# Kernel tuning notes

Hardware: AMD Instinct MI355X
Metric: run time of the kernel (lower is better)

## Reference

```python
import jax, jax.numpy as jnp
import numpy as np

B, C, T, F = 4, 96, 320, 256
BN_EPS = 1e-5


def _cbp(x, W, b, gamma, beta, mean, var, a):
    """1x1 Conv2d + BatchNorm2d (inference stats) + PReLU (single param)."""
    y = jnp.einsum('oc,bctf->botf', W, x) + b[None, :, None, None]
    scale = gamma * jax.lax.rsqrt(var + BN_EPS)
    y = (y - mean[None, :, None, None]) * scale[None, :, None, None] + beta[None, :, None, None]
    return jnp.where(y >= 0, y, a * y)


def setup_inputs() -> dict:
    key = jax.random.key(0)
    ks = jax.random.split(key, 24)
    d = {"inp": jax.random.normal(ks[0], (B, C, T, F), dtype=jnp.float32)}

    def mk_params(i, cout):
        kk = jax.random.split(ks[i], 7)
        return dict(
            W=jax.random.normal(kk[0], (cout, C), dtype=jnp.float32) / np.sqrt(C),
            b=jnp.zeros((cout,), dtype=jnp.float32),
            gamma=jnp.ones((cout,), dtype=jnp.float32) + 0.1 * jax.random.normal(kk[1], (cout,), dtype=jnp.float32),
            beta=0.1 * jax.random.normal(kk[2], (cout,), dtype=jnp.float32),
            mean=0.1 * jax.random.normal(kk[3], (cout,), dtype=jnp.float32),
            var=jax.random.uniform(kk[4], (cout,), dtype=jnp.float32) + 0.5,
            a=jnp.float32(0.25),
        )

    for tag, i, cout in (("f", 1, 3 * C), ("t", 2, 2 * C), ("p", 3, C)):
        p = mk_params(i, cout)
        for k, v in p.items():
            d[k + "_" + tag] = v
    return d


def reference(inp,
              W_f, b_f, gamma_f, beta_f, mean_f, var_f, a_f,
              W_t, b_t, gamma_t, beta_t, mean_t, var_t, a_t,
              W_p, b_p, gamma_p, beta_p, mean_p, var_p, a_p):
    c = inp.shape[1]
    scale = 1.0 / jnp.sqrt(jnp.float32(c))

    # frequency-axis attention
    f_qkv = _cbp(inp, W_f, b_f, gamma_f, beta_f, mean_f, var_f, a_f)  # [B,3C,T,F]
    qf, kf, v = f_qkv[:, :c], f_qkv[:, c:2 * c], f_qkv[:, 2 * c:]
    f_score = jnp.einsum('bctf,bcty->btfy', qf, kf) * scale
    f_score = jax.nn.softmax(f_score, axis=-1)
    f_out = jnp.einsum('btfy,bcty->bctf', f_score, v)

    # time-axis attention (NOTE: original's masked_fill is non-inplace and
    # its result is discarded, so the causal mask has NO effect; replicated.)
    t_qk = _cbp(inp, W_t, b_t, gamma_t, beta_t, mean_t, var_t, a_t)  # [B,2C,T,F]
    qt, kt = t_qk[:, :c], t_qk[:, c:]
    t_score = jnp.einsum('bctf,bcyf->bfty', qt, kt) * scale
    t_score = jax.nn.softmax(t_score, axis=-1)
    t_out = jnp.einsum('bfty,bcyf->bctf', t_score, f_out)

    out = _cbp(t_out, W_p, b_p, gamma_p, beta_p, mean_p, var_p, a_p)
    return out + inp
```

## Files before the change

### kernel.cpp

```cpp
#include <hip/hip_runtime.h>
#include <math.h>

typedef float f4 __attribute__((ext_vector_type(4)));
typedef float f2 __attribute__((ext_vector_type(2)));
typedef float f32x4 __attribute__((ext_vector_type(4)));
typedef _Float16 h8 __attribute__((ext_vector_type(8)));

constexpr int B_ = 4, C_ = 96, T_ = 320, F_ = 256;
constexpr int TF_ = T_ * F_;
constexpr float EPS_ = 1e-5f;
constexpr size_t QH_ = (size_t)C_ * TF_;

constexpr int WPP = 92160, WTOT = 110592;

__global__ __launch_bounds__(256)
void prep_kernel(const float* __restrict__ Wf, const float* __restrict__ Wt,
                 const float* __restrict__ Wp,
                 const float* __restrict__ bf, const float* __restrict__ gf,
                 const float* __restrict__ bef, const float* __restrict__ mf,
                 const float* __restrict__ vf,
                 const float* __restrict__ bt, const float* __restrict__ gt,
                 const float* __restrict__ bet, const float* __restrict__ mt,
                 const float* __restrict__ vt,
                 const float* __restrict__ bp, const float* __restrict__ gp,
                 const float* __restrict__ bep, const float* __restrict__ mp,
                 const float* __restrict__ vp,
                 _Float16* __restrict__ wsp, float* __restrict__ scsh)
{
    const int gtid = blockIdx.x * 256 + threadIdx.x;
    const int gsz  = gridDim.x * 256;
    for (int i = gtid; i < 46080; i += gsz) {
        const int frid = i >> 9, le = i & 511;
        const int lane = le >> 3, j = le & 7;
        const int kk = frid % 3, m = (frid / 3) % 3,
                  wm = (frid / 9) & 1, cg = frid / 18;
        const int row = (wm * 3 + m) * 16 + (lane & 15);
        const int col = kk * 32 + (lane >> 4) * 8 + j;
        const float* src = (cg < 3) ? Wf + cg * 9216 : Wt + (cg - 3) * 9216;
        const float w = src[row * 96 + col];
        const _Float16 h = (_Float16)w;
        wsp[(frid * 2 + 0) * 512 + le] = h;
        wsp[(frid * 2 + 1) * 512 + le] = (_Float16)(w - (float)h);
    }
    for (int i = gtid; i < 9216; i += gsz) {
        const int frid = i >> 9, le = i & 511;
        const int lane = le >> 3, j = le & 7;
        const int kk = frid % 3, m = (frid / 3) % 3, wm = frid / 9;
        const int row = (wm * 3 + m) * 16 + (lane & 15);
        const int col = kk * 32 + (lane >> 4) * 8 + j;
        const float w = Wp[row * 96 + col];
        const _Float16 h = (_Float16)w;
        wsp[WPP + (frid * 2 + 0) * 512 + le] = h;
        wsp[WPP + (frid * 2 + 1) * 512 + le] = (_Float16)(w - (float)h);
    }
    if (gtid < 288) {
        const float sc = gf[gtid] * rsqrtf(vf[gtid] + EPS_);
        scsh[2 * gtid] = sc;
        scsh[2 * gtid + 1] = fmaf(bf[gtid] - mf[gtid], sc, bef[gtid]);
    } else if (gtid < 480) {
        const int i = gtid - 288;
        const float sc = gt[i] * rsqrtf(vt[i] + EPS_);
        scsh[576 + 2 * i] = sc;
        scsh[576 + 2 * i + 1] = fmaf(bt[i] - mt[i], sc, bet[i]);
    } else if (gtid < 576) {
        const int i = gtid - 480;
        const float sc = gp[i] * rsqrtf(vp[i] + EPS_);
        scsh[960 + 2 * i] = sc;
        scsh[960 + 2 * i + 1] = fmaf(bp[i] - mp[i], sc, bep[i]);
    }
}

__global__ __launch_bounds__(256, 3)
void conv_ft(const float* __restrict__ x, const _Float16* __restrict__ wsp,
             const float* __restrict__ scsh,
             const float* __restrict__ aPf, const float* __restrict__ aPt,
             _Float16* __restrict__ yf, _Float16* __restrict__ yt,
             int bsx, int bsyf, int bsyt)
{
    constexpr int LS = 200;
    extern __shared__ _Float16 ldsh[];
    _Float16* Xs0 = ldsh;
    _Float16* Xs1 = ldsh + 64 * LS;

    x  += (size_t)blockIdx.y * bsx;
    yf += (size_t)blockIdx.y * bsyf;
    yt += (size_t)blockIdx.y * bsyt;

    const int tid = threadIdx.x;
    const int p0A = blockIdx.x * 128;
    const int p0B = p0A + 64;

    {
        const float* xg = x + p0A;
        for (int e = tid; e < 64 * 12; e += 256) {
            const int p = e & 63, k0 = (e >> 6) * 8;
            const float* xp = xg + (size_t)k0 * TF_ + p;
            h8 hv, lv;
#pragma unroll
            for (int j = 0; j < 8; ++j) {
                const float xv = xp[(size_t)j * TF_];
                const _Float16 xh = (_Float16)xv;
                hv[j] = xh;
                lv[j] = (_Float16)(xv - (float)xh);
            }
            *(h8*)&Xs0[p * LS + k0]      = hv;
            *(h8*)&Xs0[p * LS + 96 + k0] = lv;
        }
    }

    const int lane = tid & 63, wid = tid >> 6;
    const int l16 = lane & 15, lg = lane >> 4;
    const int wm = wid >> 1, wn = wid & 1;
    const float af_ = aPf[0], at_ = aPt[0];
    __syncthreads();

    float xpre[3][8];
#pragma unroll
    for (int it = 0; it < 3; ++it) {
        const int e = tid + it * 256;
        const int p = e & 63, k0 = (e >> 6) * 8;
        const float* xp = x + p0B + (size_t)k0 * TF_ + p;
#pragma unroll
        for (int j = 0; j < 8; ++j) xpre[it][j] = xp[(size_t)j * TF_];
    }

    auto compute5 = [&](const _Float16* Xs, int p0) {
#pragma unroll 1
        for (int cg = 0; cg < 5; ++cg) {
            const float* ss; float a; _Float16* yo;
            if (cg < 3) {
                ss = scsh + cg * 192;        a = af_;
                yo = yf + (size_t)cg * QH_;
            } else {
                ss = scsh + 576 + (cg - 3) * 192;  a = at_;
                yo = yt + (size_t)(cg - 3) * QH_;
            }
            const _Float16* wbase = wsp + (size_t)(cg * 2 + wm) * 9 * 1024 + lane * 8;

            f32x4 acc[3][2];
#pragma unroll
            for (int m = 0; m < 3; ++m)
#pragma unroll
                for (int n = 0; n < 2; ++n) acc[m][n] = (f32x4){0.f, 0.f, 0.f, 0.f};

#pragma unroll
            for (int kk = 0; kk < 3; ++kk) {
                h8 bfh[2], bfl[2];
#pragma unroll
                for (int n = 0; n < 2; ++n) {
                    const int prow = (wn * 2 + n) * 16 + l16;
                    bfh[n] = *(const h8*)&Xs[prow * LS + kk * 32 + lg * 8];
                    bfl[n] = *(const h8*)&Xs[prow * LS + 96 + kk * 32 + lg * 8];
                }
#pragma unroll
                for (int m = 0; m < 3; ++m) {
                    const _Float16* wr = wbase + (size_t)(m * 3 + kk) * 1024;
                    const h8 wh = *(const h8*)&wr[0];
                    const h8 wl = *(const h8*)&wr[512];
#pragma unroll
                    for (int n = 0; n < 2; ++n) {
                        acc[m][n] = __builtin_amdgcn_mfma_f32_16x16x32_f16(wh, bfh[n], acc[m][n], 0, 0, 0);
                        acc[m][n] = __builtin_amdgcn_mfma_f32_16x16x32_f16(wl, bfh[n], acc[m][n], 0, 0, 0);
                        acc[m][n] = __builtin_amdgcn_mfma_f32_16x16x32_f16(wh, bfl[n], acc[m][n], 0, 0, 0);
                    }
                }
            }

#pragma unroll
            for (int m = 0; m < 3; ++m) {
#pragma unroll
                for (int r = 0; r < 4; ++r) {
                    const int col = (wm * 3 + m) * 16 + lg * 4 + r;
                    const f2 sp = *(const f2*)&ss[2 * col];
                    _Float16* yr = yo + (size_t)col * TF_ + p0 + wn * 32 + l16;
#pragma unroll
                    for (int n = 0; n < 2; ++n) {
                        const float v = fmaf(acc[m][n][r], sp[0], sp[1]);
                        yr[n * 16] = (_Float16)(v >= 0.f ? v : a * v);
                    }
                }
            }
        }
    };

    compute5(Xs0, p0A);

#pragma unroll
    for (int it = 0; it < 3; ++it) {
        const int e = tid + it * 256;
        const int p = e & 63, k0 = (e >> 6) * 8;
        h8 hv, lv;
#pragma unroll
        for (int j = 0; j < 8; ++j) {
            const _Float16 xh = (_Float16)xpre[it][j];
            hv[j] = xh;
            lv[j] = (_Float16)(xpre[it][j] - (float)xh);
        }
        *(h8*)&Xs1[p * LS + k0]      = hv;
        *(h8*)&Xs1[p * LS + 96 + k0] = lv;
    }
    __syncthreads();

    compute5(Xs1, p0B);
}

__device__ __forceinline__ void tr64_body(const _Float16* __restrict__ in,
                                          _Float16* __restrict__ out,
                                          int Mo, int No, int n0, int m0,
                                          _Float16* tile)
{
    const int t = threadIdx.x, ty = t >> 3, tx8 = t & 7;
#pragma unroll
    for (int r = 0; r < 2; ++r) {
        const int n = ty + r * 32;
        const h8 v = *(const h8*)&in[(size_t)(n0 + n) * Mo + m0 + tx8 * 8];
        const int c = tx8 ^ (n >> 3);
        *(h8*)&tile[n * 72 + c * 8] = v;
    }
    __syncthreads();
#pragma unroll
    for (int r = 0; r < 2; ++r) {
        const int mt = ty + r * 32;
        h8 v;
#pragma unroll
        for (int j = 0; j < 8; ++j) {
            const int n = tx8 * 8 + j;
            const int c = (mt >> 3) ^ tx8;
            v[j] = tile[n * 72 + c * 8 + (mt & 7)];
        }
        *(h8*)&out[(size_t)(m0 + mt) * No + n0 + tx8 * 8] = v;
    }
}

__global__ __launch_bounds__(256)
void transpose_trA(const _Float16* __restrict__ doh, _Float16* __restrict__ wsh)
{
    __shared__ _Float16 tile[64 * 72];
    const int b = blockIdx.z >> 1, t = blockIdx.z & 1;
    const _Float16* in  = t ? doh + (size_t)b * 2 * QH_
                            : wsh + (size_t)b * 3 * QH_;
    _Float16*       out = t ? wsh + (size_t)b * 3 * QH_ + 2 * QH_
                            : wsh + (size_t)b * 3 * QH_ + QH_;
    tr64_body(in, out, F_, C_ * T_, blockIdx.x * 64, blockIdx.y * 64, tile);
}

__global__ __launch_bounds__(256)
void transpose_trB(const _Float16* __restrict__ doh, _Float16* __restrict__ wsh)
{
    __shared__ _Float16 tile[64 * 72];
    const int b = blockIdx.z;
    tr64_body(doh + (size_t)b * 2 * QH_ + QH_, wsh + (size_t)b * 3 * QH_,
              F_, C_ * T_, blockIdx.x * 64, blockIdx.y * 64, tile);
}

__global__ __launch_bounds__(256)
void transpose_hf_res(const _Float16* __restrict__ in, const float* __restrict__ res,
                      float* __restrict__ out, int si, int sr, int so)
{
    __shared__ _Float16 tile[64 * 72];
    in  += (size_t)blockIdx.z * si;
    res += (size_t)blockIdx.z * sr;
    out += (size_t)blockIdx.z * so;
    const int n0 = blockIdx.x * 64, m0 = blockIdx.y * 64;
    const int t = threadIdx.x, ty = t >> 3, tx8 = t & 7;
#pragma unroll
    for (int r = 0; r < 2; ++r) {
        const int n = ty + r * 32;
        const h8 v = *(const h8*)&in[(size_t)(n0 + n) * (C_ * T_) + m0 + tx8 * 8];
        const int c = tx8 ^ (n >> 3);
        *(h8*)&tile[n * 72 + c * 8] = v;
    }
    __syncthreads();
#pragma unroll
    for (int r = 0; r < 2; ++r) {
        const int mt = ty + r * 32;
        const size_t obase = (size_t)(m0 + mt) * F_ + n0 + tx8 * 8;
        const f4 r0 = *(const f4*)&res[obase];
        const f4 r1 = *(const f4*)&res[obase + 4];
        f4 o0, o1;
#pragma unroll
        for (int j = 0; j < 8; ++j) {
            const int n = tx8 * 8 + j;
            const int c = (mt >> 3) ^ tx8;
            const float v = (float)tile[n * 72 + c * 8 + (mt & 7)];
            if (j < 4) o0[j] = v + r0[j]; else o1[j - 4] = v + r1[j - 4];
        }
        *(f4*)&out[obase]     = o0;
        *(f4*)&out[obase + 4] = o1;
    }
}

template<int MODE>
__global__ __launch_bounds__(256, 2)
void attn_mfma(const _Float16* __restrict__ Qb, const _Float16* __restrict__ Kb,
               const _Float16* __restrict__ Vb, _Float16* __restrict__ Ob,
               int qs, int ks, int vs, int os)
{
    constexpr int NY  = (MODE == 0) ? 256 : 320;
    constexpr int LD  = (MODE == 0) ? TF_ : T_;
    constexpr int NT  = NY / 16;
    constexpr int NYK = NY / 32;
    constexpr int KS  = 104;
    constexpr int VPS = (MODE == 0) ? 256 : 344;
    constexpr int KVH = (NY * KS > 96 * VPS) ? NY * KS : 96 * VPS;
    constexpr int PMS = (MODE == 0) ? 32 : 40;
    constexpr int PWO = (MODE == 0) ? 24576 : KVH;
    constexpr int NG  = (MODE == 0) ? T_ : F_;
    constexpr int GOFF = (MODE == 0) ? F_ : C_ * T_;

    extern __shared__ _Float16 ldsh[];
    _Float16* KV = ldsh;
    _Float16* Pw = ldsh + PWO;

    const int lb    = blockIdx.y;
    const int strip = blockIdx.x / NG;
    const int grp   = blockIdx.x % NG;
    const int m0    = strip * 64;
    const size_t off = (size_t)grp * GOFF;
    const _Float16* Q = Qb + (size_t)lb * qs + off;
    const _Float16* K = Kb + (size_t)lb * ks + off;
    const _Float16* V = Vb + (size_t)lb * vs + off;
    _Float16*       O = Ob + (size_t)lb * os + off;

    const int tid  = threadIdx.x;
    const int lane = tid & 63, wid = tid >> 6;
    const int l16  = lane & 15, lg = lane >> 4;
    const int mw   = wid * 16;
    const float scale = 0.10206207261596575f;

    for (int e = tid; e < NY * 12; e += 256) {
        const int yy = e % NY, k0 = (e / NY) * 8;
        const _Float16* kp = K + (size_t)k0 * LD + yy;
        h8 hv;
#pragma unroll
        for (int j = 0; j < 8; ++j) hv[j] = kp[(size_t)j * LD];
        *(h8*)&KV[yy * KS + k0] = hv;
    }

    h8 aQ[3];
#pragma unroll
    for (int kk = 0; kk < 3; ++kk) {
        const _Float16* qp = Q + (size_t)(kk * 32 + lg * 8) * LD + m0 + mw + l16;
#pragma unroll
        for (int j = 0; j < 8; ++j) aQ[kk][j] = qp[(size_t)j * LD];
    }
    __syncthreads();

    f32x4 sacc[NT];
#pragma unroll
    for (int t = 0; t < NT; ++t) sacc[t] = (f32x4){0.f, 0.f, 0.f, 0.f};
#pragma unroll
    for (int kk = 0; kk < 3; ++kk) {
#pragma unroll
        for (int t = 0; t < NT; ++t) {
            const h8 bK = *(const h8*)&KV[(t * 16 + l16) * KS + kk * 32 + lg * 8];
            sacc[t] = __builtin_amdgcn_mfma_f32_16x16x32_f16(aQ[kk], bK, sacc[t], 0, 0, 0);
        }
    }

#pragma unroll
    for (int r = 0; r < 4; ++r) {
        float mx = sacc[0][r];
#pragma unroll
        for (int t = 1; t < NT; ++t) mx = fmaxf(mx, sacc[t][r]);
        for (int d = 1; d < 16; d <<= 1) mx = fmaxf(mx, __shfl_xor(mx, d));
        float pv[NT];
        float sum = 0.f;
#pragma unroll
        for (int t = 0; t < NT; ++t) {
            pv[t] = __expf((sacc[t][r] - mx) * scale); sum += pv[t];
        }
        for (int d = 1; d < 16; d <<= 1) sum += __shfl_xor(sum, d);
        const float inv = 1.f / sum;
#pragma unroll
        for (int t = 0; t < NT; ++t) sacc[t][r] = pv[t] * inv;
    }
    __syncthreads();

    constexpr int NY8 = NY / 8;
    for (int e = tid; e < 96 * NY8; e += 256) {
        const int c = e / NY8, y8 = e - c * NY8;
        const int yc = (MODE == 0) ? (y8 ^ (c & 31)) : y8;
        *(h8*)&KV[c * VPS + yc * 8] = *(const h8*)(V + (size_t)c * LD + y8 * 8);
    }
    __syncthreads();

    _Float16* Pme = Pw + wid * (16 * PMS);
    f32x4 oacc[6];
#pragma unroll
    for (int ct = 0; ct < 6; ++ct) oacc[ct] = (f32x4){0.f, 0.f, 0.f, 0.f};

#pragma unroll
    for (int yk = 0; yk < NYK; ++yk) {
#pragma unroll
        for (int h = 0; h < 2; ++h)
#pragma unroll
            for (int r = 0; r < 4; ++r)
                Pme[(lg * 4 + r) * PMS + h * 16 + l16] = (_Float16)sacc[2 * yk + h][r];
        const h8 pf = *(const h8*)&Pme[l16 * PMS + lg * 8];
#pragma unroll
        for (int ct = 0; ct < 6; ++ct) {
            const int c = ct * 16 + l16;
            const int ch = (MODE == 0) ? ((yk * 4 + lg) ^ (c & 31)) : (yk * 4 + lg);
            const h8 av = *(const h8*)&KV[c * VPS + ch * 8];
            oacc[ct] = __builtin_amdgcn_mfma_f32_16x16x32_f16(av, pf, oacc[ct], 0, 0, 0);
        }
    }
#pragma unroll
    for (int ct = 0; ct < 6; ++ct)
#pragma unroll
        for (int r = 0; r < 4; ++r)
            O[(size_t)(ct * 16 + lg * 4 + r) * LD + m0 + mw + l16] = (_Float16)oacc[ct][r];
}

__global__ __launch_bounds__(256, 2)
void attn1_fused(const _Float16* __restrict__ Qb, const _Float16* __restrict__ Kb,
                 const _Float16* __restrict__ Vb, _Float16* __restrict__ tmpb,
                 const _Float16* __restrict__ wsp, const float* __restrict__ scsh,
                 const float* __restrict__ aPp,
                 int qs, int ks, int vs, int ts)
{
    constexpr int NY = 320, LD = T_, NT = 20, NYK = 10;
    constexpr int KS = 104, VPS = 344;
    constexpr int KVH = NY * KS;
    constexpr int OS  = 104;

    extern __shared__ _Float16 ldsh[];
    _Float16* KV = ldsh;
    _Float16* Pw = ldsh + KVH;
    _Float16* Ot = ldsh;

    const int lb    = blockIdx.y;
    const int strip = blockIdx.x / F_;
    const int grp   = blockIdx.x % F_;
    const int m0    = strip * 64;
    const size_t off = (size_t)grp * (C_ * T_);
    const _Float16* Q = Qb + (size_t)lb * qs + off;
    const _Float16* K = Kb + (size_t)lb * ks + off;
    const _Float16* V = Vb + (size_t)lb * vs + off;
    _Float16*     tmp = tmpb + (size_t)lb * ts + (size_t)grp * (96 * T_);

    const int tid  = threadIdx.x;
    const int lane = tid & 63, wid = tid >> 6;
    const int l16  = lane & 15, lg = lane >> 4;
    const int mw   = wid * 16;
    const float scale = 0.10206207261596575f;

    for (int e = tid; e < NY * 12; e += 256) {
        const int yy = e % NY, k0 = (e / NY) * 8;
        const _Float16* kp = K + (size_t)k0 * LD + yy;
        h8 hv;
#pragma unroll
        for (int j = 0; j < 8; ++j) hv[j] = kp[(size_t)j * LD];
        *(h8*)&KV[yy * KS + k0] = hv;
    }

    h8 aQ[3];
#pragma unroll
    for (int kk = 0; kk < 3; ++kk) {
        const _Float16* qp = Q + (size_t)(kk * 32 + lg * 8) * LD + m0 + mw + l16;
#pragma unroll
        for (int j = 0; j < 8; ++j) aQ[kk][j] = qp[(size_t)j * LD];
    }
    __syncthreads();

    f32x4 sacc[NT];
#pragma unroll
    for (int t = 0; t < NT; ++t) sacc[t] = (f32x4){0.f, 0.f, 0.f, 0.f};
#pragma unroll
    for (int kk = 0; kk < 3; ++kk) {
#pragma unroll
        for (int t = 0; t < NT; ++t) {
            const h8 bK = *(const h8*)&KV[(t * 16 + l16) * KS + kk * 32 + lg * 8];
            sacc[t] = __builtin_amdgcn_mfma_f32_16x16x32_f16(aQ[kk], bK, sacc[t], 0, 0, 0);
        }
    }

#pragma unroll
    for (int r = 0; r < 4; ++r) {
        float mx = sacc[0][r];
#pragma unroll
        for (int t = 1; t < NT; ++t) mx = fmaxf(mx, sacc[t][r]);
        for (int d = 1; d < 16; d <<= 1) mx = fmaxf(mx, __shfl_xor(mx, d));
        float pv[NT];
        float sum = 0.f;
#pragma unroll
        for (int t = 0; t < NT; ++t) {
            pv[t] = __expf((sacc[t][r] - mx) * scale); sum += pv[t];
        }
        for (int d = 1; d < 16; d <<= 1) sum += __shfl_xor(sum, d);
        const float inv = 1.f / sum;
#pragma unroll
        for (int t = 0; t < NT; ++t) sacc[t][r] = pv[t] * inv;
    }
    __syncthreads();

    for (int e = tid; e < 96 * 40; e += 256) {
        const int c = e / 40, y8 = e - c * 40;
        *(h8*)&KV[c * VPS + y8 * 8] = *(const h8*)(V + (size_t)c * LD + y8 * 8);
    }
    __syncthreads();

    _Float16* Pme = Pw + wid * 640;
    f32x4 oacc[6];
#pragma unroll
    for (int ct = 0; ct < 6; ++ct) oacc[ct] = (f32x4){0.f, 0.f, 0.f, 0.f};

#pragma unroll
    for (int yk = 0; yk < NYK; ++yk) {
#pragma unroll
        for (int h = 0; h < 2; ++h)
#pragma unroll
            for (int r = 0; r < 4; ++r)
                Pme[(lg * 4 + r) * 40 + h * 16 + l16] = (_Float16)sacc[2 * yk + h][r];
        const h8 pf = *(const h8*)&Pme[l16 * 40 + lg * 8];
#pragma unroll
        for (int ct = 0; ct < 6; ++ct) {
            const h8 av = *(const h8*)&KV[(ct * 16 + l16) * VPS + yk * 32 + lg * 8];
            oacc[ct] = __builtin_amdgcn_mfma_f32_16x16x32_f16(av, pf, oacc[ct], 0, 0, 0);
        }
    }

    __syncthreads();
#pragma unroll
    for (int ct = 0; ct < 6; ++ct)
#pragma unroll
        for (int r = 0; r < 4; ++r)
            Ot[(mw + l16) * OS + ct * 16 + lg * 4 + r] = (_Float16)oacc[ct][r];
    __syncthreads();

    const int wm = wid >> 1, wn = wid & 1;
    const float a = aPp[0];
    const float* ss = scsh + 960;
    const _Float16* wbase = wsp + WPP + (size_t)wm * 9 * 1024 + lane * 8;

    f32x4 acc2[3][2];
#pragma unroll
    for (int m = 0; m < 3; ++m)
#pragma unroll
        for (int n = 0; n < 2; ++n) acc2[m][n] = (f32x4){0.f, 0.f, 0.f, 0.f};

#pragma unroll
    for (int kk = 0; kk < 3; ++kk) {
        h8 bf[2];
#pragma unroll
        for (int n = 0; n < 2; ++n)
            bf[n] = *(const h8*)&Ot[((wn * 2 + n) * 16 + l16) * OS + kk * 32 + lg * 8];
#pragma unroll
        for (int m = 0; m < 3; ++m) {
            const _Float16* wr = wbase + (size_t)(m * 3 + kk) * 1024;
            const h8 wh = *(const h8*)&wr[0];
            const h8 wl = *(const h8*)&wr[512];
#pragma unroll
            for (int n = 0; n < 2; ++n) {
                acc2[m][n] = __builtin_amdgcn_mfma_f32_16x16x32_f16(wh, bf[n], acc2[m][n], 0, 0, 0);
                acc2[m][n] = __builtin_amdgcn_mfma_f32_16x16x32_f16(wl, bf[n], acc2[m][n], 0, 0, 0);
            }
        }
    }

#pragma unroll
    for (int m = 0; m < 3; ++m) {
#pragma unroll
        for (int r = 0; r < 4; ++r) {
            const int co = (wm * 3 + m) * 16 + lg * 4 + r;
            const f2 sp = *(const f2*)&ss[2 * co];
            _Float16* yr = tmp + (size_t)co * T_ + m0 + wn * 32 + l16;
#pragma unroll
            for (int n = 0; n < 2; ++n) {
                const float v = fmaf(acc2[m][n][r], sp[0], sp[1]);
                yr[n * 16] = (_Float16)(v >= 0.f ? v : a * v);
            }
        }
    }
}

extern "C" void kernel_launch(void* const* d_in, const int* in_sizes, int n_in,
                              void* d_out, int out_size, void* d_ws, size_t ws_size,
                              hipStream_t stream)
{
    const float* inp = (const float*)d_in[0];
    const float* W_f = (const float*)d_in[1];  const float* b_f = (const float*)d_in[2];
    const float* g_f = (const float*)d_in[3];  const float* be_f = (const float*)d_in[4];
    const float* m_f = (const float*)d_in[5];  const float* v_f = (const float*)d_in[6];
    const float* a_f = (const float*)d_in[7];
    const float* W_t = (const float*)d_in[8];  const float* b_t = (const float*)d_in[9];
    const float* g_t = (const float*)d_in[10]; const float* be_t = (const float*)d_in[11];
    const float* m_t = (const float*)d_in[12]; const float* v_t = (const float*)d_in[13];
    const float* a_t = (const float*)d_in[14];
    const float* W_p = (const float*)d_in[15]; const float* b_p = (const float*)d_in[16];
    const float* g_p = (const float*)d_in[17]; const float* be_p = (const float*)d_in[18];
    const float* m_p = (const float*)d_in[19]; const float* v_p = (const float*)d_in[20];
    const float* a_p = (const float*)d_in[21];

    hipFuncSetAttribute((const void*)conv_ft,
                        hipFuncAttributeMaxDynamicSharedMemorySize, 51200);
    hipFuncSetAttribute((const void*)attn_mfma<0>,
                        hipFuncAttributeMaxDynamicSharedMemorySize, 53248);
    hipFuncSetAttribute((const void*)attn1_fused,
                        hipFuncAttributeMaxDynamicSharedMemorySize, 71680);

    constexpr int QH = (int)QH_;
    const size_t tail  = (size_t)WTOT * 2 + 1152 * 4 + 4096;
    const size_t need4 = (size_t)12 * QH * 2 + tail;
    const int G = (ws_size >= need4) ? 4 : 2;

    _Float16* wsh  = (_Float16*)d_ws;
    _Float16* wsp  = wsh + (size_t)3 * G * QH;
    float*    scsh = (float*)(wsp + WTOT);

    prep_kernel<<<dim3(128), dim3(256), 0, stream>>>(
        W_f, W_t, W_p, b_f, g_f, be_f, m_f, v_f,
        b_t, g_t, be_t, m_t, v_t, b_p, g_p, be_p, m_p, v_p, wsp, scsh);

    for (int p = 0; p < B_ / G; ++p) {
        const float* xb  = inp + (size_t)p * G * QH;
        float*       dob = (float*)d_out + (size_t)p * G * QH;
        _Float16*    doh = (_Float16*)dob;

        conv_ft<<<dim3(640, G), dim3(256), 51200, stream>>>(
            xb, wsp, scsh, a_f, a_t, wsh, doh, QH, 3 * QH, 2 * QH);
        attn_mfma<0><<<dim3(T_ * (F_ / 64), G), dim3(256), 53248, stream>>>(
            wsh, wsh + QH_, wsh + 2 * QH_, wsh, 3 * QH, 3 * QH, 3 * QH, 3 * QH);
        transpose_trA<<<dim3(480, 4, 2 * G), dim3(256), 0, stream>>>(doh, wsh);
        transpose_trB<<<dim3(480, 4, G), dim3(256), 0, stream>>>(doh, wsh);
        attn1_fused<<<dim3(F_ * (T_ / 64), G), dim3(256), 71680, stream>>>(
            wsh + 2 * QH_, wsh, wsh + QH_, wsh + 2 * QH_, wsp, scsh, a_p,
            3 * QH, 3 * QH, 3 * QH, 3 * QH);
        transpose_hf_res<<<dim3(4, 480, G), dim3(256), 0, stream>>>(
            wsh + 2 * QH_, xb, dob, 3 * QH, QH, QH);
    }
}
```

Baseline: 618.5 us.

## Tile time-attention keys into two chunks with online softmax

Replaces the single-pass softmax over all 320 keys in the fused time-attention kernel with a two-chunk flash-style online softmax. A running max and sum are kept and the output accumulators are rescaled between chunks. This halves the K/V shared-memory footprint (71680 to 39424 bytes) and the score registers, aiming for higher occupancy. In exchange it adds extra syncs, an extra rescale pass, and serializes the K and V loads per chunk.

```diff
diff --git a/kernel.cpp b/kernel.cpp
--- a/kernel.cpp
+++ b/kernel.cpp
@@ -420,15 +420,18 @@
                  const float* __restrict__ aPp,
                  int qs, int ks, int vs, int ts)
 {
-    constexpr int NY = 320, LD = T_, NT = 20, NYK = 10;
-    constexpr int KS = 104, VPS = 344;
-    constexpr int KVH = NY * KS;
+    constexpr int LD = T_;
+    constexpr int KT = 160;
+    constexpr int KS = 108;
+    constexpr int VPS = 172;
     constexpr int OS  = 104;
+    constexpr int PMS = 36;
+    constexpr int AREG = KT * KS;
+    constexpr int PME0 = AREG;
+    constexpr int FB0  = AREG + 4 * 16 * PMS;
 
     extern __shared__ _Float16 ldsh[];
     _Float16* KV = ldsh;
-    _Float16* Pw = ldsh + KVH;
-    _Float16* Ot = ldsh;
 
     const int lb    = blockIdx.y;
     const int strip = blockIdx.x / F_;
@@ -446,14 +449,9 @@
     const int mw   = wid * 16;
     const float scale = 0.10206207261596575f;
 
-    for (int e = tid; e < NY * 12; e += 256) {
-        const int yy = e % NY, k0 = (e / NY) * 8;
-        const _Float16* kp = K + (size_t)k0 * LD + yy;
-        h8 hv;
-#pragma unroll
-        for (int j = 0; j < 8; ++j) hv[j] = kp[(size_t)j * LD];
-        *(h8*)&KV[yy * KS + k0] = hv;
-    }
+    _Float16* Pme = ldsh + PME0 + wid * (16 * PMS);
+    float*    fbuf = (float*)(ldsh + FB0) + wid * 16;
+    _Float16* Ot = ldsh;
 
     h8 aQ[3];
 #pragma unroll
@@ -462,66 +460,102 @@
 #pragma unroll
         for (int j = 0; j < 8; ++j) aQ[kk][j] = qp[(size_t)j * LD];
     }
-    __syncthreads();
-
-    f32x4 sacc[NT];
-#pragma unroll
-    for (int t = 0; t < NT; ++t) sacc[t] = (f32x4){0.f, 0.f, 0.f, 0.f};
-#pragma unroll
-    for (int kk = 0; kk < 3; ++kk) {
-#pragma unroll
-        for (int t = 0; t < NT; ++t) {
-            const h8 bK = *(const h8*)&KV[(t * 16 + l16) * KS + kk * 32 + lg * 8];
-            sacc[t] = __builtin_amdgcn_mfma_f32_16x16x32_f16(aQ[kk], bK, sacc[t], 0, 0, 0);
-        }
-    }
-
-#pragma unroll
-    for (int r = 0; r < 4; ++r) {
-        float mx = sacc[0][r];
-#pragma unroll
-        for (int t = 1; t < NT; ++t) mx = fmaxf(mx, sacc[t][r]);
-        for (int d = 1; d < 16; d <<= 1) mx = fmaxf(mx, __shfl_xor(mx, d));
-        float pv[NT];
-        float sum = 0.f;
-#pragma unroll
-        for (int t = 0; t < NT; ++t) {
-            pv[t] = __expf((sacc[t][r] - mx) * scale); sum += pv[t];
-        }
-        for (int d = 1; d < 16; d <<= 1) sum += __shfl_xor(sum, d);
-        const float inv = 1.f / sum;
-#pragma unroll
-        for (int t = 0; t < NT; ++t) sacc[t][r] = pv[t] * inv;
-    }
-    __syncthreads();
-
-    for (int e = tid; e < 96 * 40; e += 256) {
-        const int c = e / 40, y8 = e - c * 40;
-        *(h8*)&KV[c * VPS + y8 * 8] = *(const h8*)(V + (size_t)c * LD + y8 * 8);
-    }
-    __syncthreads();
-
-    _Float16* Pme = Pw + wid * 640;
+
     f32x4 oacc[6];
 #pragma unroll
     for (int ct = 0; ct < 6; ++ct) oacc[ct] = (f32x4){0.f, 0.f, 0.f, 0.f};
-
-#pragma unroll
-    for (int yk = 0; yk < NYK; ++yk) {
-#pragma unroll
-        for (int h = 0; h < 2; ++h)
-#pragma unroll
-            for (int r = 0; r < 4; ++r)
-                Pme[(lg * 4 + r) * 40 + h * 16 + l16] = (_Float16)sacc[2 * yk + h][r];
-        const h8 pf = *(const h8*)&Pme[l16 * 40 + lg * 8];
-#pragma unroll
-        for (int ct = 0; ct < 6; ++ct) {
-            const h8 av = *(const h8*)&KV[(ct * 16 + l16) * VPS + yk * 32 + lg * 8];
-            oacc[ct] = __builtin_amdgcn_mfma_f32_16x16x32_f16(av, pf, oacc[ct], 0, 0, 0);
-        }
-    }
-
-    __syncthreads();
+    float mrun[4], lrun[4];
+#pragma unroll
+    for (int r = 0; r < 4; ++r) { mrun[r] = -1e30f; lrun[r] = 0.f; }
+
+#pragma unroll 1
+    for (int kt = 0; kt < 2; ++kt) {
+        for (int e = tid; e < KT * 12; e += 256) {
+            const int yy = e % KT, k0 = (e / KT) * 8;
+            const _Float16* kp = K + (size_t)k0 * LD + kt * KT + yy;
+            h8 hv;
+#pragma unroll
+            for (int j = 0; j < 8; ++j) hv[j] = kp[(size_t)j * LD];
+            *(h8*)&KV[yy * KS + k0] = hv;
+        }
+        __syncthreads();
+
+        f32x4 sacc[10];
+#pragma unroll
+        for (int t = 0; t < 10; ++t) sacc[t] = (f32x4){0.f, 0.f, 0.f, 0.f};
+#pragma unroll
+        for (int kk = 0; kk < 3; ++kk) {
+#pragma unroll
+            for (int t = 0; t < 10; ++t) {
+                const h8 bK = *(const h8*)&KV[(t * 16 + l16) * KS + kk * 32 + lg * 8];
+                sacc[t] = __builtin_amdgcn_mfma_f32_16x16x32_f16(aQ[kk], bK, sacc[t], 0, 0, 0);
+            }
+        }
+
+        float fr[4];
+#pragma unroll
+        for (int r = 0; r < 4; ++r) {
+            float pmax = sacc[0][r];
+#pragma unroll
+            for (int t = 1; t < 10; ++t) pmax = fmaxf(pmax, sacc[t][r]);
+            for (int d = 1; d < 16; d <<= 1) pmax = fmaxf(pmax, __shfl_xor(pmax, d));
+            const float mnew = fmaxf(mrun[r], pmax);
+            fr[r] = __expf((mrun[r] - mnew) * scale);
+            float psum = 0.f;
+#pragma unroll
+            for (int t = 0; t < 10; ++t) {
+                const float p = __expf((sacc[t][r] - mnew) * scale);
+                sacc[t][r] = p; psum += p;
+            }
+            for (int d = 1; d < 16; d <<= 1) psum += __shfl_xor(psum, d);
+            lrun[r] = lrun[r] * fr[r] + psum;
+            mrun[r] = mnew;
+        }
+        if (l16 == 0) {
+#pragma unroll
+            for (int r = 0; r < 4; ++r) fbuf[lg * 4 + r] = fr[r];
+        }
+        __syncthreads();
+
+        for (int e = tid; e < 96 * 20; e += 256) {
+            const int c = e / 20, y8 = e % 20;
+            *(h8*)&KV[c * VPS + y8 * 8] =
+                *(const h8*)(V + (size_t)c * LD + kt * KT + y8 * 8);
+        }
+        const float fl = fbuf[l16];
+#pragma unroll
+        for (int ct = 0; ct < 6; ++ct)
+#pragma unroll
+            for (int r = 0; r < 4; ++r) oacc[ct][r] *= fl;
+        __syncthreads();
+
+#pragma unroll
+        for (int yk = 0; yk < 5; ++yk) {
+#pragma unroll
+            for (int h = 0; h < 2; ++h)
+#pragma unroll
+                for (int r = 0; r < 4; ++r)
+                    Pme[(lg * 4 + r) * PMS + h * 16 + l16] = (_Float16)sacc[2 * yk + h][r];
+            const h8 pf = *(const h8*)&Pme[l16 * PMS + lg * 8];
+#pragma unroll
+            for (int ct = 0; ct < 6; ++ct) {
+                const h8 av = *(const h8*)&KV[(ct * 16 + l16) * VPS + yk * 32 + lg * 8];
+                oacc[ct] = __builtin_amdgcn_mfma_f32_16x16x32_f16(av, pf, oacc[ct], 0, 0, 0);
+            }
+        }
+        __syncthreads();
+    }
+
+    if (l16 == 0) {
+#pragma unroll
+        for (int r = 0; r < 4; ++r) fbuf[lg * 4 + r] = 1.f / lrun[r];
+    }
+    const float il = fbuf[l16];
+#pragma unroll
+    for (int ct = 0; ct < 6; ++ct)
+#pragma unroll
+        for (int r = 0; r < 4; ++r) oacc[ct][r] *= il;
+
 #pragma unroll
     for (int ct = 0; ct < 6; ++ct)
 #pragma unroll
@@ -598,7 +632,7 @@
     hipFuncSetAttribute((const void*)attn_mfma<0>,
                         hipFuncAttributeMaxDynamicSharedMemorySize, 53248);
     hipFuncSetAttribute((const void*)attn1_fused,
-                        hipFuncAttributeMaxDynamicSharedMemorySize, 71680);
+                        hipFuncAttributeMaxDynamicSharedMemorySize, 39424);
 
     constexpr int QH = (int)QH_;
     const size_t tail  = (size_t)WTOT * 2 + 1152 * 4 + 4096;
@@ -624,7 +658,7 @@
             wsh, wsh + QH_, wsh + 2 * QH_, wsh, 3 * QH, 3 * QH, 3 * QH, 3 * QH);
         transpose_trA<<<dim3(480, 4, 2 * G), dim3(256), 0, stream>>>(doh, wsh);
         transpose_trB<<<dim3(480, 4, G), dim3(256), 0, stream>>>(doh, wsh);
-        attn1_fused<<<dim3(F_ * (T_ / 64), G), dim3(256), 71680, stream>>>(
+        attn1_fused<<<dim3(F_ * (T_ / 64), G), dim3(256), 39424, stream>>>(
             wsh + 2 * QH_, wsh, wsh + QH_, wsh + 2 * QH_, wsp, scsh, a_p,
             3 * QH, 3 * QH, 3 * QH, 3 * QH);
         transpose_hf_res<<<dim3(4, 480, G), dim3(256), 0, stream>>>(
```

Result: slower. 822.1 us (+32.9%).
